# Performance work log

Measured on AMD Instinct MI355X. Metric: run time of the kernel, lower is better.

Reference implementation:

```python
import jax, jax.numpy as jnp
import numpy as np

N, M, LOC_MAX, EMB, D = 16, 100, 10000, 128, 4  # batch, max_len, n_locations, emb_dim, delta feature dim


def setup_inputs() -> dict:
    key = jax.random.key(0)
    k1, k2, k3, k4, k5 = jax.random.split(key, 5)
    return {
        "self_attn": jax.random.normal(k1, (N, M, EMB), jnp.float32),
        "self_delta": jax.random.normal(k2, (N, M, LOC_MAX, D), jnp.float32),
        "traj_len": jax.random.randint(k3, (N,), 0, M),  # unused by forward (kept for signature fidelity)
        "emb_table": jax.random.normal(k4, (LOC_MAX + 1, EMB), jnp.float32) * 0.02,
        "value_w": jax.random.normal(k5, (M,), jnp.float32) * 0.1,  # Linear(max_len, 1, bias=False) weight
    }


def reference(self_attn, self_delta, traj_len, emb_table, value_w):
    # self_delta: [N, M, L, D] -> sum last dim -> [N, M, L] -> transpose -> [N, L, M]
    delta = jnp.sum(self_delta, axis=-1).transpose(0, 2, 1)
    # candidates = 1..loc_max (same for every batch row), so gather once: [L, EMB]
    emb_cand = emb_table[1:LOC_MAX + 1]
    # bmm(emb_candidates, self_attn^T) -> [N, L, M], then elementwise decay
    attn = jnp.einsum('ld,nmd->nlm', emb_cand, self_attn) * delta
    # Linear(max_len, 1, bias=False) over last axis, view to [N, L]
    return jnp.einsum('nlm,m->nl', attn, value_w)
```

## Files before the change

### kernel.cpp

```cpp
#include <hip/hip_runtime.h>

#define N_   16
#define M_   100
#define L_   10000
#define EMB_ 128
#define TL   64
#define NT   256

__global__ __launch_bounds__(NT, 5) void attn_fused_kernel(
    const float* __restrict__ self_attn,
    const float* __restrict__ self_delta,
    const float* __restrict__ emb_table,
    const float* __restrict__ value_w,
    float* __restrict__ out)
{
    __shared__ float dltw[TL][M_ + 1];
    __shared__ float red[4][TL];
    __shared__ float wsh[M_];

    const int n   = blockIdx.y;
    const int l0  = blockIdx.x * TL;
    const int tid = threadIdx.x;

    if (tid < M_) wsh[tid] = value_w[tid];
    __syncthreads();

    const float4* dp = (const float4*)self_delta + (size_t)n * M_ * L_;
    #pragma unroll 5
    for (int it = 0; it < (TL * M_) / NT; ++it) {
        int idx = tid + it * NT;
        int ll  = idx & (TL - 1);
        int m   = idx >> 6;
        int l   = l0 + ll;
        float v = 0.f;
        if (l < L_) {
            float4 d4 = dp[(size_t)m * L_ + l];
            v = (d4.x + d4.y + d4.z + d4.w) * wsh[m];
        }
        dltw[ll][m] = v;
    }
    __syncthreads();

    const int ll    = tid & (TL - 1);
    const int chunk = __builtin_amdgcn_readfirstlane(tid >> 6);
    const int l     = l0 + ll;

    float acc[32];
    #pragma unroll
    for (int j = 0; j < 32; ++j) acc[j] = 0.f;

    const float* ap = self_attn + (size_t)n * M_ * EMB_ + chunk * 32;
    #pragma unroll 2
    for (int m = 0; m < M_; ++m) {
        float dw = dltw[ll][m];
        const float* a = ap + m * EMB_;
        #pragma unroll
        for (int j = 0; j < 32; ++j) {
            acc[j] += a[j] * dw;
        }
    }

    float part = 0.f;
    if (l < L_) {
        const float4* e = (const float4*)(emb_table + (size_t)(l + 1) * EMB_ + chunk * 32);
        #pragma unroll
        for (int j = 0; j < 8; ++j) {
            float4 ev = e[j];
            part += ev.x * acc[4 * j + 0] + ev.y * acc[4 * j + 1]
                  + ev.z * acc[4 * j + 2] + ev.w * acc[4 * j + 3];
        }
    }
    red[chunk][ll] = part;
    __syncthreads();

    if (tid < TL) {
        float r = red[0][tid] + red[1][tid] + red[2][tid] + red[3][tid];
        int lg = l0 + tid;
        if (lg < L_) out[(size_t)n * L_ + lg] = r;
    }
}

extern "C" void kernel_launch(void* const* d_in, const int* in_sizes, int n_in,
                              void* d_out, int out_size, void* d_ws, size_t ws_size,
                              hipStream_t stream) {
    const float* self_attn  = (const float*)d_in[0];
    const float* self_delta = (const float*)d_in[1];
    const float* emb_table  = (const float*)d_in[3];
    const float* value_w    = (const float*)d_in[4];
    float* out = (float*)d_out;

    dim3 grid((L_ + TL - 1) / TL, N_);
    attn_fused_kernel<<<grid, NT, 0, stream>>>(self_attn, self_delta, emb_table, value_w, out);
}
```

Baseline: 408.2 us.

## Compute delta-attn contraction with fp16 MFMA using swizzled LDS tiles

Replaces the scalar FMA loop over M with MFMA 16x16x32 fp16 matrix ops. The delta sums and the value_w-scaled self_attn are staged into swizzled, zero-padded fp16 shared-memory tiles. The final dot with emb_table now uses a per-lane gather and a cross-lane shuffle reduction instead of a shared-memory reduction. The kernel remains bound by streaming self_delta, so the compute savings may matter little, while fp16 conversion reduces precision and the block rebuilds the B tile for every L tile.

```diff
diff --git a/kernel.cpp b/kernel.cpp
--- a/kernel.cpp
+++ b/kernel.cpp
@@ -6,27 +6,48 @@
 #define EMB_ 128
 #define TL   64
 #define NT   256
+#define KP   128
 
-__global__ __launch_bounds__(NT, 5) void attn_fused_kernel(
+#define SWZ(row, k) (((((k) >> 3) ^ ((row) & 7)) << 3) | ((k) & 7))
+
+typedef _Float16 half8  __attribute__((ext_vector_type(8)));
+typedef float    floatx4 __attribute__((ext_vector_type(4)));
+
+__global__ __launch_bounds__(NT, 3) void attn_fused_kernel(
     const float* __restrict__ self_attn,
     const float* __restrict__ self_delta,
     const float* __restrict__ emb_table,
     const float* __restrict__ value_w,
     float* __restrict__ out)
 {
-    __shared__ float dltw[TL][M_ + 1];
-    __shared__ float red[4][TL];
-    __shared__ float wsh[M_];
+    __shared__ _Float16 A_s[TL * KP];
+    __shared__ _Float16 B_s[EMB_ * KP];
 
     const int n   = blockIdx.y;
     const int l0  = blockIdx.x * TL;
     const int tid = threadIdx.x;
 
-    if (tid < M_) wsh[tid] = value_w[tid];
-    __syncthreads();
+    for (int i = tid; i < 192 * 32; i += NT) {
+        int r = i >> 5, j = i & 31;
+        if (j < 28) {
+            int k = 100 + j;
+            if (r < TL) A_s[r * KP + SWZ(r, k)]        = (_Float16)0.f;
+            else        B_s[(r - TL) * KP + SWZ(r - TL, k)] = (_Float16)0.f;
+        }
+    }
+
+    const float* ap = self_attn + (size_t)n * M_ * EMB_;
+    #pragma unroll 5
+    for (int i = tid; i < M_ * EMB_; i += NT) {
+        int m = i >> 7;
+        int d = i & 127;
+        int mu = __builtin_amdgcn_readfirstlane(m);
+        float wv = value_w[mu];
+        B_s[d * KP + SWZ(d, m)] = (_Float16)(ap[i] * wv);
+    }
 
     const float4* dp = (const float4*)self_delta + (size_t)n * M_ * L_;
-    #pragma unroll 5
+    #pragma unroll
     for (int it = 0; it < (TL * M_) / NT; ++it) {
         int idx = tid + it * NT;
         int ll  = idx & (TL - 1);
@@ -35,48 +56,57 @@
         float v = 0.f;
         if (l < L_) {
             float4 d4 = dp[(size_t)m * L_ + l];
-            v = (d4.x + d4.y + d4.z + d4.w) * wsh[m];
+            v = d4.x + d4.y + d4.z + d4.w;
         }
-        dltw[ll][m] = v;
+        A_s[ll * KP + SWZ(ll, m)] = (_Float16)v;
     }
     __syncthreads();
 
-    const int ll    = tid & (TL - 1);
-    const int chunk = __builtin_amdgcn_readfirstlane(tid >> 6);
-    const int l     = l0 + ll;
+    const int lane = tid & 63;
+    const int wid  = tid >> 6;
+    const int row  = lane & 15;
+    const int q    = lane >> 4;
 
-    float acc[32];
+    floatx4 acc[8];
     #pragma unroll
-    for (int j = 0; j < 32; ++j) acc[j] = 0.f;
+    for (int t = 0; t < 8; ++t) acc[t] = (floatx4){0.f, 0.f, 0.f, 0.f};
 
-    const float* ap = self_attn + (size_t)n * M_ * EMB_ + chunk * 32;
-    #pragma unroll 2
-    for (int m = 0; m < M_; ++m) {
-        float dw = dltw[ll][m];
-        const float* a = ap + m * EMB_;
+    const int arow = wid * 16 + row;
+    #pragma unroll
+    for (int kc = 0; kc < 4; ++kc) {
+        int c = kc * 4 + q;
+        half8 a = *(const half8*)&A_s[arow * KP + ((c ^ (arow & 7)) << 3)];
         #pragma unroll
-        for (int j = 0; j < 32; ++j) {
-            acc[j] += a[j] * dw;
+        for (int t = 0; t < 8; ++t) {
+            int brow = t * 16 + row;
+            half8 b = *(const half8*)&B_s[brow * KP + ((c ^ (brow & 7)) << 3)];
+            acc[t] = __builtin_amdgcn_mfma_f32_16x16x32_f16(a, b, acc[t], 0, 0, 0);
         }
     }
 
-    float part = 0.f;
-    if (l < L_) {
-        const float4* e = (const float4*)(emb_table + (size_t)(l + 1) * EMB_ + chunk * 32);
+    float part[4] = {0.f, 0.f, 0.f, 0.f};
+    const int lbase = l0 + wid * 16 + q * 4;
+    #pragma unroll
+    for (int t = 0; t < 8; ++t) {
+        int d = t * 16 + row;
         #pragma unroll
-        for (int j = 0; j < 8; ++j) {
-            float4 ev = e[j];
-            part += ev.x * acc[4 * j + 0] + ev.y * acc[4 * j + 1]
-                  + ev.z * acc[4 * j + 2] + ev.w * acc[4 * j + 3];
+        for (int r = 0; r < 4; ++r) {
+            int lrow = lbase + r + 1;
+            if (lrow > L_) lrow = L_;
+            part[r] += acc[t][r] * emb_table[(size_t)lrow * EMB_ + d];
         }
     }
-    red[chunk][ll] = part;
-    __syncthreads();
-
-    if (tid < TL) {
-        float r = red[0][tid] + red[1][tid] + red[2][tid] + red[3][tid];
-        int lg = l0 + tid;
-        if (lg < L_) out[(size_t)n * L_ + lg] = r;
+    #pragma unroll
+    for (int off = 1; off < 16; off <<= 1) {
+        #pragma unroll
+        for (int r = 0; r < 4; ++r) part[r] += __shfl_xor(part[r], off);
+    }
+    if (row == 0) {
+        #pragma unroll
+        for (int r = 0; r < 4; ++r) {
+            int l = lbase + r;
+            if (l < L_) out[(size_t)n * L_ + l] = part[r];
+        }
     }
 }
 
```

Measured after the change: 436.3 us. +6.9%, slower.
